# Kernel tuning notes

Measured on AMD Instinct MI355X. Metric: run time of the kernel, lower is better.

## Reference

```python
import jax, jax.numpy as jnp
import numpy as np

DIM = 768
HEADS = 12
HEAD_DIM = DIM // HEADS
EPS = 1e-5


def layernorm(x, gamma, beta):
    mu = jnp.mean(x, axis=-1, keepdims=True)
    var = jnp.var(x, axis=-1, keepdims=True)
    return (x - mu) * jax.lax.rsqrt(var + EPS) * gamma + beta


def setup_inputs() -> dict:
    key = jax.random.key(0)
    ks = jax.random.split(key, 9)
    B, N, C = 4, 2048, DIM
    s_in = 1.0 / np.sqrt(C)
    return {
        "x": jax.random.normal(ks[0], (B, N, C), dtype=jnp.float32),
        "qkv_w": jax.random.normal(ks[1], (3 * C, C), dtype=jnp.float32) * s_in,
        "qkv_b": jnp.zeros((3 * C,), dtype=jnp.float32),
        "proj_w": jax.random.normal(ks[2], (C, C), dtype=jnp.float32) * s_in,
        "proj_b": jnp.zeros((C,), dtype=jnp.float32),
        "q_gamma": jnp.ones((HEAD_DIM,), dtype=jnp.float32),
        "q_beta": jnp.zeros((HEAD_DIM,), dtype=jnp.float32),
        "k_gamma": jnp.ones((HEAD_DIM,), dtype=jnp.float32),
        "k_beta": jnp.zeros((HEAD_DIM,), dtype=jnp.float32),
    }


def reference(x, qkv_w, qkv_b, proj_w, proj_b, q_gamma, q_beta, k_gamma, k_beta):
    B, N, C = x.shape
    H, Dh = HEADS, C // HEADS
    scale = Dh ** (-0.5)
    # qkv projection: [B,N,3C] -> [3,B,H,N,Dh]
    qkv = (x @ qkv_w.T + qkv_b).reshape(B, N, 3, H, Dh).transpose(2, 0, 3, 1, 4)
    q, k, v = qkv[0], qkv[1], qkv[2]
    q = layernorm(q, q_gamma, q_beta)
    k = layernorm(k, k_gamma, k_beta)
    # explicit full score matrix [B,H,N,N] as in the original module
    attn = jnp.einsum("bhqd,bhkd->bhqk", q, k) * scale
    attn = jax.nn.softmax(attn, axis=-1)
    out = jnp.einsum("bhqk,bhkd->bhqd", attn, v)  # [B,H,N,Dh]
    out = out.transpose(0, 2, 1, 3).reshape(B, N, C)
    return out @ proj_w.T + proj_b
```

## Files before the change

### kernel.cpp

```cpp
#include <hip/hip_runtime.h>
#include <hip/hip_bf16.h>
#include <cstdint>
#include <cstddef>

#define BB 4
#define SEQ 2048
#define CD 768
#define NH 12
#define DH 64
#define MROWS (BB*SEQ)
#define NQKV (3*CD)

typedef float f32x4 __attribute__((ext_vector_type(4)));
typedef float f32x16 __attribute__((ext_vector_type(16)));
typedef short bf16x8 __attribute__((ext_vector_type(8)));

static __device__ __forceinline__ unsigned short f2bf(float f) {
  union { float f; unsigned int u; } cv; cv.f = f;
  unsigned int u = cv.u;
  unsigned int r = (u + 0x7FFFu + ((u >> 16) & 1u)) >> 16;
  return (unsigned short)r;
}

static __device__ __forceinline__ float fexp2(float x) {
#if __has_builtin(__builtin_amdgcn_exp2f)
  return __builtin_amdgcn_exp2f(x);
#else
  float r; asm("v_exp_f32 %0, %1" : "=v"(r) : "v"(x)); return r;
#endif
}

#define GAS __attribute__((address_space(1)))
#define LAS __attribute__((address_space(3)))
static __device__ __forceinline__ void gl2lds16(const void* g, void* l) {
  __builtin_amdgcn_global_load_lds((const GAS void*)g, (LAS void*)l, 16, 0, 0);
}

#define MFMA(a, b, c) __builtin_amdgcn_mfma_f32_16x16x32_bf16((a), (b), (c), 0, 0, 0)
#define MFMA32(a, b, c) __builtin_amdgcn_mfma_f32_32x32x16_bf16((a), (b), (c), 0, 0, 0)
#define PACKBF(dst, x, y) asm("v_cvt_pk_bf16_f32 %0, %1, %2" : "=v"(dst) : "v"(x), "v"(y))
#define SWAP32(a, b) asm("v_permlane32_swap_b32 %0, %1" : "+v"(a), "+v"(b))

#define QSC 0.18033688011112042f

__global__ __launch_bounds__(256) void cvt_bf16(const float* __restrict__ in,
                                                unsigned short* __restrict__ out, int n4) {
  int i = blockIdx.x * 256 + threadIdx.x;
  if (i >= n4) return;
  float4 v = reinterpret_cast<const float4*>(in)[i];
  unsigned int lo = (unsigned int)f2bf(v.x) | ((unsigned int)f2bf(v.y) << 16);
  unsigned int hi = (unsigned int)f2bf(v.z) | ((unsigned int)f2bf(v.w) << 16);
  reinterpret_cast<uint2*>(out)[i] = make_uint2(lo, hi);
}

__global__ __launch_bounds__(256) void qkv_gemm(
    const unsigned short* __restrict__ Xb, const unsigned short* __restrict__ Wb,
    const float* __restrict__ bias,
    const float* __restrict__ qg, const float* __restrict__ qbt,
    const float* __restrict__ kg, const float* __restrict__ kbt,
    unsigned short* __restrict__ Qo, unsigned short* __restrict__ Ko,
    unsigned short* __restrict__ Vt) {
  __shared__ unsigned short As[2][128 * 32];
  __shared__ unsigned short Bs[2][128 * 32];
  const int tid = threadIdx.x;
  const int wave = tid >> 6, lane = tid & 63;
  const int g = lane >> 4, cl = lane & 15;
  const int bm = blockIdx.x, bn = blockIdx.y;
  const int wr = (wave >> 1) * 64, wc = (wave & 1) * 64;

  f32x4 acc[4][4] = {};

  const int kc = (tid & 3) * 8;
  const unsigned short* ag0 = Xb + (size_t)(bm * 128 + (tid >> 2)) * CD + kc;
  const unsigned short* ag1 = ag0 + (size_t)64 * CD;
  const unsigned short* bg0 = Wb + (size_t)(bn * 128 + (tid >> 2)) * CD + kc;
  const unsigned short* bg1 = bg0 + (size_t)64 * CD;

#define QSTAGE(buf, k0)                             \
  do {                                              \
    gl2lds16(ag0 + (k0), &As[buf][tid * 8]);        \
    gl2lds16(ag1 + (k0), &As[buf][tid * 8 + 2048]); \
    gl2lds16(bg0 + (k0), &Bs[buf][tid * 8]);        \
    gl2lds16(bg1 + (k0), &Bs[buf][tid * 8 + 2048]); \
  } while (0)

  QSTAGE(0, 0);
  __syncthreads();
  const int NIT = CD / 32;
  for (int it = 0; it < NIT; ++it) {
    const int cur = it & 1;
    if (it + 1 < NIT) QSTAGE(cur ^ 1, (it + 1) * 32);
    bf16x8 af[4], bfr[4];
#pragma unroll
    for (int i = 0; i < 4; ++i) af[i] = *(const bf16x8*)&As[cur][(wr + i * 16 + cl) * 32 + g * 8];
#pragma unroll
    for (int j = 0; j < 4; ++j) bfr[j] = *(const bf16x8*)&Bs[cur][(wc + j * 16 + cl) * 32 + g * 8];
#pragma unroll
    for (int i = 0; i < 4; ++i)
#pragma unroll
      for (int j = 0; j < 4; ++j) acc[i][j] = MFMA(af[i], bfr[j], acc[i][j]);
    __syncthreads();
  }
#undef QSTAGE

  const int j0 = bn * 128 + wc;
  const int t = j0 / CD;
  const int h = (j0 % CD) / DH;
  float bia[4], gam[4] = {0, 0, 0, 0}, bet[4] = {0, 0, 0, 0};
#pragma unroll
  for (int j = 0; j < 4; ++j) {
    int d = j * 16 + cl;
    bia[j] = bias[j0 + d];
    if (t == 0) { gam[j] = qg[d] * QSC; bet[j] = qbt[d] * QSC; }
    else if (t == 1) { gam[j] = kg[d]; bet[j] = kbt[d]; }
  }

  if (t == 2) {
#pragma unroll
    for (int i = 0; i < 4; ++i) {
      const int mrow = bm * 128 + wr + i * 16 + g * 4;
      const int b = mrow >> 11, nn = mrow & 2047;
#pragma unroll
      for (int j = 0; j < 4; ++j) {
        const int d = j * 16 + cl;
        unsigned int lo = (unsigned int)f2bf(acc[i][j][0] + bia[j]) |
                          ((unsigned int)f2bf(acc[i][j][1] + bia[j]) << 16);
        unsigned int hi2 = (unsigned int)f2bf(acc[i][j][2] + bia[j]) |
                           ((unsigned int)f2bf(acc[i][j][3] + bia[j]) << 16);
        *reinterpret_cast<uint2*>(&Vt[((size_t)(b * NH + h) * DH + d) * SEQ + nn]) =
            make_uint2(lo, hi2);
      }
    }
    return;
  }

  unsigned short* Out = (t == 0) ? Qo : Ko;
#pragma unroll
  for (int i = 0; i < 4; ++i) {
#pragma unroll
    for (int r = 0; r < 4; ++r) {
      float vj[4];
#pragma unroll
      for (int j = 0; j < 4; ++j) vj[j] = acc[i][j][r] + bia[j];
      const int m = bm * 128 + wr + i * 16 + g * 4 + r;
      const int b = m >> 11, n = m & 2047;
      size_t base = ((size_t)(b * NH + h) * SEQ + n) * DH;
      float s = vj[0] + vj[1] + vj[2] + vj[3];
      float ss = vj[0] * vj[0] + vj[1] * vj[1] + vj[2] * vj[2] + vj[3] * vj[3];
#pragma unroll
      for (int msk = 1; msk < 16; msk <<= 1) {
        s += __shfl_xor(s, msk, 64);
        ss += __shfl_xor(ss, msk, 64);
      }
      float mu = s * (1.0f / 64.0f);
      float var = ss * (1.0f / 64.0f) - mu * mu;
      float rstd = rsqrtf(var + 1e-5f);
#pragma unroll
      for (int j = 0; j < 4; ++j)
        Out[base + j * 16 + cl] = f2bf((vj[j] - mu) * rstd * gam[j] + bet[j]);
    }
  }
}

__global__ __launch_bounds__(256, 3) void attn_fwd(
    const unsigned short* __restrict__ Qb, const unsigned short* __restrict__ Kb,
    const unsigned short* __restrict__ Vtb, unsigned short* __restrict__ Ob) {
  __shared__ unsigned short kl[2][64 * 64];
  __shared__ unsigned short vt[2][64 * 64];
  const int tid = threadIdx.x, wave = tid >> 6, lane = tid & 63;
  const int q32 = lane & 31, hi = lane >> 5;

  const int wg = blockIdx.x;
  const int lin = (wg & 7) * 96 + (wg >> 3);
  const int bh = lin >> 4;
  const int qbase = (lin & 15) * 128 + wave * 32;

  const unsigned short* qrow = Qb + ((size_t)bh * SEQ + qbase + q32) * DH + hi * 8;
  bf16x8 qf[4];
#pragma unroll
  for (int dc = 0; dc < 4; ++dc) qf[dc] = *(const bf16x8*)&qrow[dc * 16];

  const unsigned short* Kh = Kb + (size_t)bh * SEQ * DH;
  const unsigned short* Vth = Vtb + (size_t)bh * DH * SEQ;

  const int sr = tid >> 3;
  const int sc = 8 * ((tid & 7) ^ (sr & 7));
  const int ksw = (q32 & 7) << 3;

  const short oneb = (short)0x3F80;
  const bf16x8 onesv = {oneb, oneb, oneb, oneb, oneb, oneb, oneb, oneb};

#define ASTAGE(buf, kb0)                                                      \
  do {                                                                        \
    gl2lds16(&Kh[(size_t)((kb0) + sr) * DH + sc], &kl[buf][tid * 8]);         \
    gl2lds16(&Kh[(size_t)((kb0) + sr + 32) * DH + sc], &kl[buf][tid * 8 + 2048]); \
    gl2lds16(&Vth[(size_t)sr * SEQ + (kb0) + sc], &vt[buf][tid * 8]);         \
    gl2lds16(&Vth[(size_t)(sr + 32) * SEQ + (kb0) + sc], &vt[buf][tid * 8 + 2048]); \
  } while (0)

  f32x16 o0 = {}, o1 = {}, ol = {};

  ASTAGE(0, 0);
  __syncthreads();
  const int NT = SEQ / 64;
#pragma unroll 2
  for (int it = 0; it < NT; ++it) {
    const int cur = it & 1;
    if (it + 1 < NT) ASTAGE(cur ^ 1, (it + 1) * 64);

    f32x16 s0 = {}, s1 = {};
    __builtin_amdgcn_s_setprio(1);
#pragma unroll
    for (int dc = 0; dc < 4; ++dc) {
      const int colb = dc * 16 + hi * 8;
      bf16x8 kf0 = *(const bf16x8*)&kl[cur][q32 * 64 + (colb ^ ksw)];
      bf16x8 kf1 = *(const bf16x8*)&kl[cur][(32 + q32) * 64 + (colb ^ ksw)];
      s0 = MFMA32(kf0, qf[dc], s0);
      s1 = MFMA32(kf1, qf[dc], s1);
    }
    __builtin_amdgcn_s_setprio(0);

#pragma unroll
    for (int r = 0; r < 16; ++r) {
      s0[r] = fexp2(s0[r]);
      s1[r] = fexp2(s1[r]);
    }

    bf16x8 pav[4];
#pragma unroll
    for (int c = 0; c < 4; ++c) {
      const int b = 8 * (c & 1);
      unsigned int wA0, wA1, wB0, wB1;
      if (c < 2) {
        PACKBF(wA0, s0[b + 0], s0[b + 1]); PACKBF(wA1, s0[b + 2], s0[b + 3]);
        PACKBF(wB0, s0[b + 4], s0[b + 5]); PACKBF(wB1, s0[b + 6], s0[b + 7]);
      } else {
        PACKBF(wA0, s1[b + 0], s1[b + 1]); PACKBF(wA1, s1[b + 2], s1[b + 3]);
        PACKBF(wB0, s1[b + 4], s1[b + 5]); PACKBF(wB1, s1[b + 6], s1[b + 7]);
      }
      SWAP32(wA0, wB0);
      SWAP32(wA1, wB1);
      union { unsigned int w[4]; bf16x8 v; } u;
      u.w[0] = wA0; u.w[1] = wA1; u.w[2] = wB0; u.w[3] = wB1;
      pav[c] = u.v;
    }

    __builtin_amdgcn_s_setprio(1);
#pragma unroll
    for (int c = 0; c < 4; ++c) {
      const int colb = c * 16 + hi * 8;
      bf16x8 vf0 = *(const bf16x8*)&vt[cur][q32 * 64 + (colb ^ ksw)];
      bf16x8 vf1 = *(const bf16x8*)&vt[cur][(32 + q32) * 64 + (colb ^ ksw)];
      o0 = MFMA32(pav[c], vf0, o0);
      o1 = MFMA32(pav[c], vf1, o1);
      ol = MFMA32(pav[c], onesv, ol);
    }
    __builtin_amdgcn_s_setprio(0);
    __syncthreads();
  }
#undef ASTAGE

  const int b = bh / NH, h = bh % NH;
#pragma unroll
  for (int r = 0; r < 16; ++r) {
    const int qq = (r & 3) + 8 * (r >> 2) + 4 * hi;
    const float iv = __builtin_amdgcn_rcpf(ol[r]);
    size_t base = ((size_t)(b * SEQ + qbase + qq)) * CD + h * DH;
    Ob[base + q32] = f2bf(o0[r] * iv);
    Ob[base + 32 + q32] = f2bf(o1[r] * iv);
  }
}

__global__ __launch_bounds__(256) void proj_gemm(
    const unsigned short* __restrict__ Ab, const unsigned short* __restrict__ Wb,
    const float* __restrict__ bias, float* __restrict__ out) {
  __shared__ unsigned short As[2][128 * 32];
  __shared__ unsigned short Bs[2][128 * 32];
  const int tid = threadIdx.x;
  const int wave = tid >> 6, lane = tid & 63;
  const int g = lane >> 4, cl = lane & 15;
  const int bm = blockIdx.x, bn = blockIdx.y;
  const int wr = (wave >> 1) * 64, wc = (wave & 1) * 64;

  f32x4 acc[4][4] = {};

  const int kc = (tid & 3) * 8;
  const unsigned short* ag0 = Ab + (size_t)(bm * 128 + (tid >> 2)) * CD + kc;
  const unsigned short* ag1 = ag0 + (size_t)64 * CD;
  const unsigned short* bg0 = Wb + (size_t)(bn * 128 + (tid >> 2)) * CD + kc;
  const unsigned short* bg1 = bg0 + (size_t)64 * CD;

#define PSTAGE(buf, k0)                             \
  do {                                              \
    gl2lds16(ag0 + (k0), &As[buf][tid * 8]);        \
    gl2lds16(ag1 + (k0), &As[buf][tid * 8 + 2048]); \
    gl2lds16(bg0 + (k0), &Bs[buf][tid * 8]);        \
    gl2lds16(bg1 + (k0), &Bs[buf][tid * 8 + 2048]); \
  } while (0)

  PSTAGE(0, 0);
  __syncthreads();
  const int NIT = CD / 32;
  for (int it = 0; it < NIT; ++it) {
    const int cur = it & 1;
    if (it + 1 < NIT) PSTAGE(cur ^ 1, (it + 1) * 32);
    bf16x8 af[4], bfr[4];
#pragma unroll
    for (int i = 0; i < 4; ++i) af[i] = *(const bf16x8*)&As[cur][(wr + i * 16 + cl) * 32 + g * 8];
#pragma unroll
    for (int j = 0; j < 4; ++j) bfr[j] = *(const bf16x8*)&Bs[cur][(wc + j * 16 + cl) * 32 + g * 8];
#pragma unroll
    for (int i = 0; i < 4; ++i)
#pragma unroll
      for (int j = 0; j < 4; ++j) acc[i][j] = MFMA(af[i], bfr[j], acc[i][j]);
    __syncthreads();
  }
#undef PSTAGE

  const int j0 = bn * 128 + wc;
  float pb4[4];
#pragma unroll
  for (int j = 0; j < 4; ++j) pb4[j] = bias[j0 + j * 16 + cl];
#pragma unroll
  for (int i = 0; i < 4; ++i) {
#pragma unroll
    for (int r = 0; r < 4; ++r) {
      const int m = bm * 128 + wr + i * 16 + g * 4 + r;
      float* orow = out + (size_t)m * CD + j0;
#pragma unroll
      for (int j = 0; j < 4; ++j) orow[j * 16 + cl] = acc[i][j][r] + pb4[j];
    }
  }
}

extern "C" void kernel_launch(void* const* d_in, const int* in_sizes, int n_in,
                              void* d_out, int out_size, void* d_ws, size_t ws_size,
                              hipStream_t stream) {
  const float* x = (const float*)d_in[0];
  const float* qkv_w = (const float*)d_in[1];
  const float* qkv_b = (const float*)d_in[2];
  const float* proj_w = (const float*)d_in[3];
  const float* proj_b = (const float*)d_in[4];
  const float* q_gamma = (const float*)d_in[5];
  const float* q_beta = (const float*)d_in[6];
  const float* k_gamma = (const float*)d_in[7];
  const float* k_beta = (const float*)d_in[8];
  float* out = (float*)d_out;

  char* w = (char*)d_ws;
  unsigned short* Xb = (unsigned short*)w; w += (size_t)MROWS * CD * 2;
  unsigned short* Wq = (unsigned short*)w; w += (size_t)NQKV * CD * 2;
  unsigned short* Wp = (unsigned short*)w; w += (size_t)CD * CD * 2;
  unsigned short* Qo = (unsigned short*)w; w += (size_t)BB * NH * SEQ * DH * 2;
  unsigned short* Ko = (unsigned short*)w; w += (size_t)BB * NH * SEQ * DH * 2;
  unsigned short* Vt = (unsigned short*)w; w += (size_t)BB * NH * SEQ * DH * 2;
  unsigned short* Ob = (unsigned short*)w; w += (size_t)MROWS * CD * 2;

  cvt_bf16<<<MROWS * CD / 1024, 256, 0, stream>>>(x, Xb, MROWS * CD / 4);
  cvt_bf16<<<NQKV * CD / 1024, 256, 0, stream>>>(qkv_w, Wq, NQKV * CD / 4);
  cvt_bf16<<<CD * CD / 1024, 256, 0, stream>>>(proj_w, Wp, CD * CD / 4);

  qkv_gemm<<<dim3(MROWS / 128, NQKV / 128), 256, 0, stream>>>(
      Xb, Wq, qkv_b, q_gamma, q_beta, k_gamma, k_beta, Qo, Ko, Vt);

  attn_fwd<<<SEQ / 128 * BB * NH, 256, 0, stream>>>(Qo, Ko, Vt, Ob);

  proj_gemm<<<dim3(MROWS / 128, CD / 128), 256, 0, stream>>>(Ob, Wp, proj_b, out);
}
```

Before: 161.9 us.

## Enlarge QKV GEMM tiles to 256x256 with swizzled LDS and XCD-aware block mapping

The QKV GEMM moves to 256x256 output tiles with 512 threads, a K-step of 64, XOR-swizzled LDS layouts, a block-index remap that spreads tiles across XCDs, and s_setprio around the MFMA loop. The projection GEMM gets the same K=64 step, swizzle and setprio treatment. The aim is more data reuse per global load, fewer LDS bank conflicts and fewer barriers per K. In exchange it uses much more LDS and registers (128KB LDS and 32 accumulators per lane in the QKV kernel), which may limit occupancy.

```diff
diff --git a/kernel.cpp b/kernel.cpp
--- a/kernel.cpp
+++ b/kernel.cpp
@@ -53,57 +53,76 @@
   reinterpret_cast<uint2*>(out)[i] = make_uint2(lo, hi);
 }
 
-__global__ __launch_bounds__(256) void qkv_gemm(
+__global__ __launch_bounds__(512, 2) void qkv_gemm(
     const unsigned short* __restrict__ Xb, const unsigned short* __restrict__ Wb,
     const float* __restrict__ bias,
     const float* __restrict__ qg, const float* __restrict__ qbt,
     const float* __restrict__ kg, const float* __restrict__ kbt,
     unsigned short* __restrict__ Qo, unsigned short* __restrict__ Ko,
     unsigned short* __restrict__ Vt) {
-  __shared__ unsigned short As[2][128 * 32];
-  __shared__ unsigned short Bs[2][128 * 32];
+  __shared__ unsigned short Als[2][256 * 64];
+  __shared__ unsigned short Bls[2][256 * 64];
   const int tid = threadIdx.x;
-  const int wave = tid >> 6, lane = tid & 63;
+  const int wid = tid >> 6, lane = tid & 63;
   const int g = lane >> 4, cl = lane & 15;
-  const int bm = blockIdx.x, bn = blockIdx.y;
-  const int wr = (wave >> 1) * 64, wc = (wave & 1) * 64;
-
-  f32x4 acc[4][4] = {};
-
-  const int kc = (tid & 3) * 8;
-  const unsigned short* ag0 = Xb + (size_t)(bm * 128 + (tid >> 2)) * CD + kc;
-  const unsigned short* ag1 = ag0 + (size_t)64 * CD;
-  const unsigned short* bg0 = Wb + (size_t)(bn * 128 + (tid >> 2)) * CD + kc;
-  const unsigned short* bg1 = bg0 + (size_t)64 * CD;
-
-#define QSTAGE(buf, k0)                             \
-  do {                                              \
-    gl2lds16(ag0 + (k0), &As[buf][tid * 8]);        \
-    gl2lds16(ag1 + (k0), &As[buf][tid * 8 + 2048]); \
-    gl2lds16(bg0 + (k0), &Bs[buf][tid * 8]);        \
-    gl2lds16(bg1 + (k0), &Bs[buf][tid * 8 + 2048]); \
+  const int wm = wid >> 2, wn = wid & 3;
+
+  const int wg = blockIdx.x;
+  const int wgid = (wg & 7) * 36 + (wg >> 3);
+  const int bm = wgid / 9, bn = wgid % 9;
+
+  f32x4 acc[8][4] = {};
+
+  const int srow = tid >> 3;
+  const int scol = ((tid & 7) ^ (srow & 7)) * 8;
+  const unsigned short* Abase = Xb + (size_t)(bm * 256 + srow) * CD + scol;
+  const unsigned short* Bbase = Wb + (size_t)(bn * 256 + srow) * CD + scol;
+
+#define STG(buf, kt)                                                          \
+  do {                                                                        \
+    gl2lds16(Abase + (size_t)0 * 64 * CD + (kt) * 64, &Als[buf][0 * 4096 + tid * 8]); \
+    gl2lds16(Abase + (size_t)1 * 64 * CD + (kt) * 64, &Als[buf][1 * 4096 + tid * 8]); \
+    gl2lds16(Abase + (size_t)2 * 64 * CD + (kt) * 64, &Als[buf][2 * 4096 + tid * 8]); \
+    gl2lds16(Abase + (size_t)3 * 64 * CD + (kt) * 64, &Als[buf][3 * 4096 + tid * 8]); \
+    gl2lds16(Bbase + (size_t)0 * 64 * CD + (kt) * 64, &Bls[buf][0 * 4096 + tid * 8]); \
+    gl2lds16(Bbase + (size_t)1 * 64 * CD + (kt) * 64, &Bls[buf][1 * 4096 + tid * 8]); \
+    gl2lds16(Bbase + (size_t)2 * 64 * CD + (kt) * 64, &Bls[buf][2 * 4096 + tid * 8]); \
+    gl2lds16(Bbase + (size_t)3 * 64 * CD + (kt) * 64, &Bls[buf][3 * 4096 + tid * 8]); \
   } while (0)
 
-  QSTAGE(0, 0);
+  STG(0, 0);
   __syncthreads();
-  const int NIT = CD / 32;
-  for (int it = 0; it < NIT; ++it) {
-    const int cur = it & 1;
-    if (it + 1 < NIT) QSTAGE(cur ^ 1, (it + 1) * 32);
-    bf16x8 af[4], bfr[4];
-#pragma unroll
-    for (int i = 0; i < 4; ++i) af[i] = *(const bf16x8*)&As[cur][(wr + i * 16 + cl) * 32 + g * 8];
-#pragma unroll
-    for (int j = 0; j < 4; ++j) bfr[j] = *(const bf16x8*)&Bs[cur][(wc + j * 16 + cl) * 32 + g * 8];
-#pragma unroll
-    for (int i = 0; i < 4; ++i)
-#pragma unroll
-      for (int j = 0; j < 4; ++j) acc[i][j] = MFMA(af[i], bfr[j], acc[i][j]);
+  const int NKT = CD / 64;
+  for (int kt = 0; kt < NKT; ++kt) {
+    const int cur = kt & 1;
+    if (kt + 1 < NKT) STG(cur ^ 1, kt + 1);
+    bf16x8 bfr[4][2];
+#pragma unroll
+    for (int j = 0; j < 4; ++j) {
+      const int Bcol = wn * 64 + j * 16 + cl;
+      const int sw = (Bcol & 7) << 3;
+      bfr[j][0] = *(const bf16x8*)&Bls[cur][Bcol * 64 + ((g * 8) ^ sw)];
+      bfr[j][1] = *(const bf16x8*)&Bls[cur][Bcol * 64 + ((32 + g * 8) ^ sw)];
+    }
+    __builtin_amdgcn_s_setprio(1);
+#pragma unroll
+    for (int i = 0; i < 8; ++i) {
+      const int Arow = wm * 128 + i * 16 + cl;
+      const int sw = (Arow & 7) << 3;
+      bf16x8 a0 = *(const bf16x8*)&Als[cur][Arow * 64 + ((g * 8) ^ sw)];
+      bf16x8 a1 = *(const bf16x8*)&Als[cur][Arow * 64 + ((32 + g * 8) ^ sw)];
+#pragma unroll
+      for (int j = 0; j < 4; ++j) {
+        acc[i][j] = MFMA(a0, bfr[j][0], acc[i][j]);
+        acc[i][j] = MFMA(a1, bfr[j][1], acc[i][j]);
+      }
+    }
+    __builtin_amdgcn_s_setprio(0);
     __syncthreads();
   }
-#undef QSTAGE
-
-  const int j0 = bn * 128 + wc;
+#undef STG
+
+  const int j0 = bn * 256 + wn * 64;
   const int t = j0 / CD;
   const int h = (j0 % CD) / DH;
   float bia[4], gam[4] = {0, 0, 0, 0}, bet[4] = {0, 0, 0, 0};
@@ -117,8 +136,8 @@
 
   if (t == 2) {
 #pragma unroll
-    for (int i = 0; i < 4; ++i) {
-      const int mrow = bm * 128 + wr + i * 16 + g * 4;
+    for (int i = 0; i < 8; ++i) {
+      const int mrow = bm * 256 + wm * 128 + i * 16 + g * 4;
       const int b = mrow >> 11, nn = mrow & 2047;
 #pragma unroll
       for (int j = 0; j < 4; ++j) {
@@ -136,13 +155,13 @@
 
   unsigned short* Out = (t == 0) ? Qo : Ko;
 #pragma unroll
-  for (int i = 0; i < 4; ++i) {
+  for (int i = 0; i < 8; ++i) {
 #pragma unroll
     for (int r = 0; r < 4; ++r) {
       float vj[4];
 #pragma unroll
       for (int j = 0; j < 4; ++j) vj[j] = acc[i][j][r] + bia[j];
-      const int m = bm * 128 + wr + i * 16 + g * 4 + r;
+      const int m = bm * 256 + wm * 128 + i * 16 + g * 4 + r;
       const int b = m >> 11, n = m & 2047;
       size_t base = ((size_t)(b * NH + h) * SEQ + n) * DH;
       float s = vj[0] + vj[1] + vj[2] + vj[3];
@@ -274,48 +293,64 @@
 __global__ __launch_bounds__(256) void proj_gemm(
     const unsigned short* __restrict__ Ab, const unsigned short* __restrict__ Wb,
     const float* __restrict__ bias, float* __restrict__ out) {
-  __shared__ unsigned short As[2][128 * 32];
-  __shared__ unsigned short Bs[2][128 * 32];
+  __shared__ unsigned short Als[2][128 * 64];
+  __shared__ unsigned short Bls[2][128 * 64];
   const int tid = threadIdx.x;
-  const int wave = tid >> 6, lane = tid & 63;
+  const int wid = tid >> 6, lane = tid & 63;
   const int g = lane >> 4, cl = lane & 15;
   const int bm = blockIdx.x, bn = blockIdx.y;
-  const int wr = (wave >> 1) * 64, wc = (wave & 1) * 64;
+  const int wr = (wid >> 1) * 64, wc = (wid & 1) * 64;
 
   f32x4 acc[4][4] = {};
 
-  const int kc = (tid & 3) * 8;
-  const unsigned short* ag0 = Ab + (size_t)(bm * 128 + (tid >> 2)) * CD + kc;
-  const unsigned short* ag1 = ag0 + (size_t)64 * CD;
-  const unsigned short* bg0 = Wb + (size_t)(bn * 128 + (tid >> 2)) * CD + kc;
-  const unsigned short* bg1 = bg0 + (size_t)64 * CD;
-
-#define PSTAGE(buf, k0)                             \
-  do {                                              \
-    gl2lds16(ag0 + (k0), &As[buf][tid * 8]);        \
-    gl2lds16(ag1 + (k0), &As[buf][tid * 8 + 2048]); \
-    gl2lds16(bg0 + (k0), &Bs[buf][tid * 8]);        \
-    gl2lds16(bg1 + (k0), &Bs[buf][tid * 8 + 2048]); \
+  const int srow = tid >> 3;
+  const int scol = ((tid & 7) ^ (srow & 7)) * 8;
+  const unsigned short* Abase = Ab + (size_t)(bm * 128 + srow) * CD + scol;
+  const unsigned short* Bbase = Wb + (size_t)(bn * 128 + srow) * CD + scol;
+
+#define PSTG(buf, kt)                                                         \
+  do {                                                                        \
+    gl2lds16(Abase + (size_t)0 * 32 * CD + (kt) * 64, &Als[buf][0 * 2048 + tid * 8]); \
+    gl2lds16(Abase + (size_t)1 * 32 * CD + (kt) * 64, &Als[buf][1 * 2048 + tid * 8]); \
+    gl2lds16(Abase + (size_t)2 * 32 * CD + (kt) * 64, &Als[buf][2 * 2048 + tid * 8]); \
+    gl2lds16(Abase + (size_t)3 * 32 * CD + (kt) * 64, &Als[buf][3 * 2048 + tid * 8]); \
+    gl2lds16(Bbase + (size_t)0 * 32 * CD + (kt) * 64, &Bls[buf][0 * 2048 + tid * 8]); \
+    gl2lds16(Bbase + (size_t)1 * 32 * CD + (kt) * 64, &Bls[buf][1 * 2048 + tid * 8]); \
+    gl2lds16(Bbase + (size_t)2 * 32 * CD + (kt) * 64, &Bls[buf][2 * 2048 + tid * 8]); \
+    gl2lds16(Bbase + (size_t)3 * 32 * CD + (kt) * 64, &Bls[buf][3 * 2048 + tid * 8]); \
   } while (0)
 
-  PSTAGE(0, 0);
+  PSTG(0, 0);
   __syncthreads();
-  const int NIT = CD / 32;
-  for (int it = 0; it < NIT; ++it) {
-    const int cur = it & 1;
-    if (it + 1 < NIT) PSTAGE(cur ^ 1, (it + 1) * 32);
-    bf16x8 af[4], bfr[4];
-#pragma unroll
-    for (int i = 0; i < 4; ++i) af[i] = *(const bf16x8*)&As[cur][(wr + i * 16 + cl) * 32 + g * 8];
-#pragma unroll
-    for (int j = 0; j < 4; ++j) bfr[j] = *(const bf16x8*)&Bs[cur][(wc + j * 16 + cl) * 32 + g * 8];
-#pragma unroll
-    for (int i = 0; i < 4; ++i)
-#pragma unroll
-      for (int j = 0; j < 4; ++j) acc[i][j] = MFMA(af[i], bfr[j], acc[i][j]);
+  const int NKT = CD / 64;
+  for (int kt = 0; kt < NKT; ++kt) {
+    const int cur = kt & 1;
+    if (kt + 1 < NKT) PSTG(cur ^ 1, kt + 1);
+    bf16x8 bfr[4][2];
+#pragma unroll
+    for (int j = 0; j < 4; ++j) {
+      const int Bcol = wc + j * 16 + cl;
+      const int sw = (Bcol & 7) << 3;
+      bfr[j][0] = *(const bf16x8*)&Bls[cur][Bcol * 64 + ((g * 8) ^ sw)];
+      bfr[j][1] = *(const bf16x8*)&Bls[cur][Bcol * 64 + ((32 + g * 8) ^ sw)];
+    }
+    __builtin_amdgcn_s_setprio(1);
+#pragma unroll
+    for (int i = 0; i < 4; ++i) {
+      const int Arow = wr + i * 16 + cl;
+      const int sw = (Arow & 7) << 3;
+      bf16x8 a0 = *(const bf16x8*)&Als[cur][Arow * 64 + ((g * 8) ^ sw)];
+      bf16x8 a1 = *(const bf16x8*)&Als[cur][Arow * 64 + ((32 + g * 8) ^ sw)];
+#pragma unroll
+      for (int j = 0; j < 4; ++j) {
+        acc[i][j] = MFMA(a0, bfr[j][0], acc[i][j]);
+        acc[i][j] = MFMA(a1, bfr[j][1], acc[i][j]);
+      }
+    }
+    __builtin_amdgcn_s_setprio(0);
     __syncthreads();
   }
-#undef PSTAGE
+#undef PSTG
 
   const int j0 = bn * 128 + wc;
   float pb4[4];
@@ -360,7 +395,7 @@
   cvt_bf16<<<NQKV * CD / 1024, 256, 0, stream>>>(qkv_w, Wq, NQKV * CD / 4);
   cvt_bf16<<<CD * CD / 1024, 256, 0, stream>>>(proj_w, Wp, CD * CD / 4);
 
-  qkv_gemm<<<dim3(MROWS / 128, NQKV / 128), 256, 0, stream>>>(
+  qkv_gemm<<<(MROWS / 256) * (NQKV / 256), 512, 0, stream>>>(
       Xb, Wq, qkv_b, q_gamma, q_beta, k_gamma, k_beta, Qo, Ko, Vt);
 
   attn_fwd<<<SEQ / 128 * BB * NH, 256, 0, stream>>>(Qo, Ko, Vt, Ob);
```

Result: faster. 156.3 us (-3.4%).
